# Optimization experiments

Hardware: AMD Instinct MI355X
Metric: run time of the kernel (lower is better)

Reference implementation:

```python
import jax, jax.numpy as jnp
import numpy as np

N, F, E = 1024, 32, 20


def setup_inputs() -> dict:
    key = jax.random.key(0)
    ks = jax.random.split(key, 18)
    f32 = jnp.float32
    nrm = lambda k, shape, s=1.0: (jax.random.normal(k, shape, f32) * s)
    scalar = nrm(ks[0], (N, 1, F))
    vector = nrm(ks[1], (N, 3, F))
    expansion = nrm(ks[2], (N, N, E))
    d = nrm(ks[3], (N, N, 3))
    direction = d / (jnp.linalg.norm(d, axis=-1, keepdims=True) + 1e-6)
    mask = (jax.random.uniform(ks[4], (N, N, 1)) < 0.9).astype(f32)
    w = 0.1  # weight scale
    return {
        "scalar": scalar, "vector": vector, "expansion": expansion,
        "direction": direction, "mask": mask,
        # message.msg_left: Linear(F,F) -> SiLU -> Linear(F,3F)
        "mL_w1": nrm(ks[5], (F, F), w), "mL_b1": jnp.zeros((F,), f32),
        "mL_w2": nrm(ks[6], (F, 3 * F), w), "mL_b2": jnp.zeros((3 * F,), f32),
        # message.msg_right: Linear(E, 3F)
        "mR_w": nrm(ks[7], (E, 3 * F), w), "mR_b": jnp.zeros((3 * F,), f32),
        # update.upd_right: Linear(2F,F) -> SiLU -> Linear(F,3F)
        "uR_w1": nrm(ks[8], (2 * F, F), w), "uR_b1": jnp.zeros((F,), f32),
        "uR_w2": nrm(ks[9], (F, 3 * F), w), "uR_b2": jnp.zeros((3 * F,), f32),
        # update.U / update.V: Linear(F,F,bias=False)
        "U_w": nrm(ks[10], (F, F), w),
        "V_w": nrm(ks[11], (F, F), w),
    }


def _message(s, v, expansion, direction, mask,
             mL_w1, mL_b1, mL_w2, mL_b2, mR_w, mR_b):
    # msg_left(s): [N,1,F] -> [N,1,3F]
    left = jax.nn.silu(s @ mL_w1 + mL_b1) @ mL_w2 + mL_b2
    # msg_right(expansion): [N,N,E] -> [N,N,3F] -> [N,N,1,3F]
    right = (expansion @ mR_w + mR_b)[..., None, :]
    prod = left * right                      # [N,N,1,3F]
    a, b, c = jnp.split(prod, 3, axis=-1)    # each [N,N,1,F]
    mask_ = mask[..., None]                  # [N,N,1,1]
    delta_s = jnp.sum(mask_ * b, axis=-3)    # [N,1,F]
    dv = v * a + direction[..., None] * c    # [N,N,3,F]
    delta_v = jnp.sum(mask_ * dv, axis=-3)   # [N,3,F]
    return delta_s, delta_v


def _update(scalar, vector, uR_w1, uR_b1, uR_w2, uR_b2, U_w, V_w):
    left = vector @ U_w                      # [N,3,F]
    right = vector @ V_w                     # [N,3,F]
    right_norm = jnp.linalg.norm(right, axis=-2, keepdims=True)   # [N,1,F]
    feats = jnp.concatenate((scalar, right_norm), axis=-1)        # [N,1,2F]
    feats = jax.nn.silu(feats @ uR_w1 + uR_b1) @ uR_w2 + uR_b2    # [N,1,3F]
    a, b, c = jnp.split(feats, 3, axis=-1)
    delta_v = a * left                                            # [N,3,F]
    inner = jnp.sum(left * right, axis=-2, keepdims=True)         # [N,1,F]
    delta_s = inner * b + c
    return delta_s, delta_v


def reference(scalar, vector, expansion, direction, mask,
              mL_w1, mL_b1, mL_w2, mL_b2, mR_w, mR_b,
              uR_w1, uR_b1, uR_w2, uR_b2, U_w, V_w):
    ds, dv = _message(scalar, vector, expansion, direction, mask,
                      mL_w1, mL_b1, mL_w2, mL_b2, mR_w, mR_b)
    scalar = scalar + ds
    vector = vector + dv
    ds, dv = _update(scalar, vector, uR_w1, uR_b1, uR_w2, uR_b2, U_w, V_w)
    return scalar + ds, vector + dv
```

## Files before the change

kernel.cpp:

```cpp
#include <hip/hip_runtime.h>
#include <hip/hip_bf16.h>
#include <math.h>

#define NN 1024
#define JS 64
#define NSL 16
#define PB 72
#define LP 40
#define WBUF 5376

typedef __attribute__((ext_vector_type(8))) short v8s;
typedef __attribute__((ext_vector_type(4))) float v4f;

#define MFMA(a, b, c) __builtin_amdgcn_mfma_f32_16x16x32_bf16((a), (b), (c), 0, 0, 0)

static __device__ __forceinline__ float silu_f(float x) {
    return x / (1.0f + __expf(-x));
}
static __device__ __forceinline__ unsigned short f2bf(float x) {
    __hip_bfloat16 h = __float2bfloat16(x);
    unsigned short u; __builtin_memcpy(&u, &h, 2); return u;
}
static __device__ __forceinline__ unsigned pack2bf(float lo, float hi) {
    __hip_bfloat162 h = __float22bfloat162_rn(make_float2(lo, hi));
    unsigned u; __builtin_memcpy(&u, &h, 4); return u;
}

extern "C" __global__ __launch_bounds__(128)
void node_kernel(const float* __restrict__ scalar,
                 const float* __restrict__ vector,
                 const float* __restrict__ mL_w1, const float* __restrict__ mL_b1,
                 const float* __restrict__ mL_w2, const float* __restrict__ mL_b2,
                 unsigned short* __restrict__ RT)
{
    const int j = blockIdx.x;
    const int t = threadIdx.x;
    __shared__ float ss[32], sh[32], sleft[96];

    if (t < 32) ss[t] = scalar[j * 32 + t];
    __syncthreads();
    if (t < 32) {
        float a = mL_b1[t];
        #pragma unroll
        for (int k = 0; k < 32; k++) a = fmaf(ss[k], mL_w1[k * 32 + t], a);
        sh[t] = silu_f(a);
    }
    __syncthreads();
    if (t < 96) {
        float a = mL_b2[t];
        #pragma unroll
        for (int k = 0; k < 32; k++) a = fmaf(sh[k], mL_w2[k * 96 + t], a);
        sleft[t] = a;
    }
    __syncthreads();
    for (int n = t; n < 160; n += 128) {
        float val;
        if (n < 32)        val = sleft[32 + n];
        else if (n < 128)  val = vector[j * 96 + (n - 32)] * sleft[(n - 32) & 31];
        else               val = sleft[64 + (n - 128)];
        RT[(size_t)n * NN + j] = f2bf(val);
    }
}

extern "C" __global__ __launch_bounds__(256, 3)
void edge_mfma_kernel(const float* __restrict__ expansion,
                      const float* __restrict__ direction,
                      const float* __restrict__ mask,
                      const float* __restrict__ mR_w, const float* __restrict__ mR_b,
                      const unsigned short* __restrict__ RT,
                      float* __restrict__ part)
{
    const int t = threadIdx.x;
    const int wave = t >> 6;
    const int lane = t & 63;
    const int lrow = lane & 15;
    const int quad = lane >> 4;
    const int jp = lane >> 2;
    const int g  = lane & 3;
    const int jl = jp * 2;

    const int bx = blockIdx.x;
    const int slice = bx & 15;
    const int i0 = (bx >> 4) * 4;
    const int j0s = slice * JS;

    __shared__ __align__(16) unsigned short BSm[160 * PB];
    __shared__ __align__(16) char Wm[4 * WBUF];

    for (int u = t; u < 160 * 8; u += 256) {
        const int row = u >> 3, seg = u & 7;
        *(uint4*)(BSm + row * PB + seg * 8) =
            *(const uint4*)(RT + (size_t)row * NN + j0s + seg * 8);
    }
    __syncthreads();

    char* wbase = Wm + wave * WBUF;
    const int ibase = i0 + (wave >> 1) * 2;

    if ((wave & 1) == 0) {
        unsigned short* L1 = (unsigned short*)wbase;
        float* S = (float*)wbase;

        v4f acc[16];
        #pragma unroll
        for (int q = 0; q < 16; ++q) acc[q] = (v4f){0.f, 0.f, 0.f, 0.f};

        float4 fa, fb, ca, cb; float m0, m1;
        {
            const size_t jg = (size_t)ibase * NN + j0s + jl;
            fa = *(const float4*)(expansion + jg * 20 + 4 * g);
            fb = *(const float4*)(expansion + (jg + 1) * 20 + 4 * g);
            ca = *(const float4*)(expansion + jg * 20 + 16);
            cb = *(const float4*)(expansion + (jg + 1) * 20 + 16);
            m0 = mask[jg]; m1 = mask[jg + 1];
        }

        for (int it = 0; it < 2; ++it) {
            const int i = ibase + it;
            for (int ch = 0; ch < 2; ++ch) {
                {
                    const float ea[4] = {fa.x, fa.y, fa.z, fa.w};
                    const float eb[4] = {fb.x, fb.y, fb.z, fb.w};
                    #pragma unroll
                    for (int k = 0; k < 4; ++k)
                        *(unsigned*)(L1 + (4 * g + k) * LP + jl) =
                            pack2bf(m0 * ea[k], m1 * eb[k]);
                    if (g == 3) {
                        const float caa[4] = {ca.x, ca.y, ca.z, ca.w};
                        const float cbb[4] = {cb.x, cb.y, cb.z, cb.w};
                        #pragma unroll
                        for (int k = 0; k < 4; ++k)
                            *(unsigned*)(L1 + (16 + k) * LP + jl) =
                                pack2bf(m0 * caa[k], m1 * cbb[k]);
                    }
                    if (g == 0) *(unsigned*)(L1 + 20 * LP + jl) = pack2bf(m0, m1);
                }
                {
                    const int u = it * 2 + ch;
                    const int un = (u < 3) ? u + 1 : 3;
                    const size_t jg =
                        (size_t)(ibase + (un >> 1)) * NN + j0s + (un & 1) * 32 + jl;
                    fa = *(const float4*)(expansion + jg * 20 + 4 * g);
                    fb = *(const float4*)(expansion + (jg + 1) * 20 + 4 * g);
                    ca = *(const float4*)(expansion + jg * 20 + 16);
                    cb = *(const float4*)(expansion + (jg + 1) * 20 + 16);
                    m0 = mask[jg]; m1 = mask[jg + 1];
                }
                {
                    const int ko = quad * 8;
                    const int kl = ch * 32 + ko;
                    const v8s a0 = *(const v8s*)(L1 + lrow * LP + ko);
                    const v8s a1 = *(const v8s*)(L1 + (16 + lrow) * LP + ko);
                    #pragma unroll
                    for (int nt = 0; nt < 8; ++nt) {
                        const v8s b = *(const v8s*)(BSm + (nt * 16 + lrow) * PB + kl);
                        acc[nt]     = MFMA(a0, b, acc[nt]);
                        acc[8 + nt] = MFMA(a1, b, acc[8 + nt]);
                    }
                }
            }
            float* pdst = part + ((size_t)i * NSL + slice) * 224;
            #pragma unroll
            for (int h = 0; h < 2; ++h) {
                #pragma unroll
                for (int mt = 0; mt < 2; ++mt)
                #pragma unroll
                for (int q = 0; q < 4; ++q)
                #pragma unroll
                for (int r = 0; r < 4; ++r) {
                    const int row = mt * 16 + quad * 4 + r;
                    if (row <= 20) S[row * 64 + q * 16 + lrow] = acc[mt * 8 + h * 4 + q][r];
                }
                const int col = h * 64 + lane;
                const int fw = (col < 32) ? (32 + col) : ((col - 32) & 31);
                float v = mR_b[fw] * S[20 * 64 + lane];
                #pragma unroll
                for (int e = 0; e < 20; ++e)
                    v = fmaf(mR_w[e * 96 + fw], S[e * 64 + lane], v);
                pdst[col] = v;
            }
            #pragma unroll
            for (int q = 0; q < 16; ++q) acc[q] = (v4f){0.f, 0.f, 0.f, 0.f};
        }
    } else {
        unsigned short* L2 = (unsigned short*)wbase;
        float* S = (float*)wbase;

        v4f acc[8];
        #pragma unroll
        for (int q = 0; q < 8; ++q) acc[q] = (v4f){0.f, 0.f, 0.f, 0.f};

        float4 fa, fb, ca, cb;
        float m0, m1, da0, da1, da2, db0, db1, db2;
        {
            const size_t jg = (size_t)ibase * NN + j0s + jl;
            fa = *(const float4*)(expansion + jg * 20 + 4 * g);
            fb = *(const float4*)(expansion + (jg + 1) * 20 + 4 * g);
            ca = *(const float4*)(expansion + jg * 20 + 16);
            cb = *(const float4*)(expansion + (jg + 1) * 20 + 16);
            m0 = mask[jg]; m1 = mask[jg + 1];
            da0 = direction[jg * 3 + 0]; da1 = direction[jg * 3 + 1]; da2 = direction[jg * 3 + 2];
            db0 = direction[(jg + 1) * 3 + 0]; db1 = direction[(jg + 1) * 3 + 1]; db2 = direction[(jg + 1) * 3 + 2];
        }

        for (int it = 0; it < 2; ++it) {
            const int i = ibase + it;
            for (int ch = 0; ch < 2; ++ch) {
                {
                    const float pa[3] = {m0 * da0, m0 * da1, m0 * da2};
                    const float pb[3] = {m1 * db0, m1 * db1, m1 * db2};
                    const float ea[4] = {fa.x, fa.y, fa.z, fa.w};
                    const float eb[4] = {fb.x, fb.y, fb.z, fb.w};
                    #pragma unroll
                    for (int d = 0; d < 3; ++d)
                        #pragma unroll
                        for (int k = 0; k < 4; ++k)
                            *(unsigned*)(L2 + (d * 20 + 4 * g + k) * LP + jl) =
                                pack2bf(pa[d] * ea[k], pb[d] * eb[k]);
                    if (g < 3) {
                        const float sa = (g == 0) ? pa[0] : ((g == 1) ? pa[1] : pa[2]);
                        const float sb = (g == 0) ? pb[0] : ((g == 1) ? pb[1] : pb[2]);
                        const float caa[4] = {ca.x, ca.y, ca.z, ca.w};
                        const float cbb[4] = {cb.x, cb.y, cb.z, cb.w};
                        #pragma unroll
                        for (int k = 0; k < 4; ++k)
                            *(unsigned*)(L2 + (g * 20 + 16 + k) * LP + jl) =
                                pack2bf(sa * caa[k], sb * cbb[k]);
                    } else {
                        *(unsigned*)(L2 + (60 + 0) * LP + jl) = pack2bf(pa[0], pb[0]);
                        *(unsigned*)(L2 + (60 + 1) * LP + jl) = pack2bf(pa[1], pb[1]);
                        *(unsigned*)(L2 + (60 + 2) * LP + jl) = pack2bf(pa[2], pb[2]);
                    }
                }
                {
                    const int u = it * 2 + ch;
                    const int un = (u < 3) ? u + 1 : 3;
                    const size_t jg =
                        (size_t)(ibase + (un >> 1)) * NN + j0s + (un & 1) * 32 + jl;
                    fa = *(const float4*)(expansion + jg * 20 + 4 * g);
                    fb = *(const float4*)(expansion + (jg + 1) * 20 + 4 * g);
                    ca = *(const float4*)(expansion + jg * 20 + 16);
                    cb = *(const float4*)(expansion + (jg + 1) * 20 + 16);
                    m0 = mask[jg]; m1 = mask[jg + 1];
                    da0 = direction[jg * 3 + 0]; da1 = direction[jg * 3 + 1]; da2 = direction[jg * 3 + 2];
                    db0 = direction[(jg + 1) * 3 + 0]; db1 = direction[(jg + 1) * 3 + 1]; db2 = direction[(jg + 1) * 3 + 2];
                }
                {
                    const int ko = quad * 8;
                    const int kl = ch * 32 + ko;
                    const v8s c0 = *(const v8s*)(L2 + (lrow) * LP + ko);
                    const v8s c1 = *(const v8s*)(L2 + (16 + lrow) * LP + ko);
                    const v8s c2 = *(const v8s*)(L2 + (32 + lrow) * LP + ko);
                    const v8s c3 = *(const v8s*)(L2 + (48 + lrow) * LP + ko);
                    const v8s b0 = *(const v8s*)(BSm + (128 + lrow) * PB + kl);
                    const v8s b1 = *(const v8s*)(BSm + (144 + lrow) * PB + kl);
                    acc[0] = MFMA(c0, b0, acc[0]); acc[1] = MFMA(c0, b1, acc[1]);
                    acc[2] = MFMA(c1, b0, acc[2]); acc[3] = MFMA(c1, b1, acc[3]);
                    acc[4] = MFMA(c2, b0, acc[4]); acc[5] = MFMA(c2, b1, acc[5]);
                    acc[6] = MFMA(c3, b0, acc[6]); acc[7] = MFMA(c3, b1, acc[7]);
                }
            }
            float* pdst = part + ((size_t)i * NSL + slice) * 224;
            #pragma unroll
            for (int h2 = 0; h2 < 2; ++h2) {
                #pragma unroll
                for (int mt = 0; mt < 4; ++mt)
                #pragma unroll
                for (int r = 0; r < 4; ++r) {
                    const int row = mt * 16 + quad * 4 + r;
                    if (row <= 62) S[row * 16 + lrow] = acc[mt * 2 + h2][r];
                }
                if (lane < 48) {
                    const int dd = lane >> 4, f16 = lane & 15;
                    const int f = h2 * 16 + f16;
                    float v = mR_b[64 + f] * S[(60 + dd) * 16 + f16];
                    #pragma unroll
                    for (int e = 0; e < 20; ++e)
                        v = fmaf(mR_w[e * 96 + 64 + f], S[(dd * 20 + e) * 16 + f16], v);
                    pdst[128 + dd * 32 + f] = v;
                }
            }
            #pragma unroll
            for (int q = 0; q < 8; ++q) acc[q] = (v4f){0.f, 0.f, 0.f, 0.f};
        }
    }
}

extern "C" __global__ __launch_bounds__(256)
void combine_kernel(const float* __restrict__ scalar,
                    const float* __restrict__ vector,
                    const float* __restrict__ uR_w1, const float* __restrict__ uR_b1,
                    const float* __restrict__ uR_w2, const float* __restrict__ uR_b2,
                    const float* __restrict__ U_w,  const float* __restrict__ V_w,
                    const float* __restrict__ part,
                    float* __restrict__ out)
{
    const int i = blockIdx.x;
    const int t = threadIdx.x;
    __shared__ float pcomb[224];
    __shared__ float snew[32], vnew[96];
    __shared__ float lU[96], rV[96], rnorm[32], h2[32], f2[96];

    if (t < 224) {
        const float* p = part + (size_t)i * NSL * 224 + t;
        float a = 0.f;
        #pragma unroll
        for (int s = 0; s < NSL; ++s) a += p[s * 224];
        pcomb[t] = a;
    }
    __syncthreads();

    if (t < 128) {
        const int d = t >> 5, ff = t & 31;
        if (d == 0) snew[ff] = scalar[i * 32 + ff] + pcomb[ff];
        else {
            const int q = t - 32;
            vnew[q] = vector[i * 96 + q] + pcomb[32 + q] + pcomb[128 + q];
        }
    }
    __syncthreads();

    if (t < 96) {
        const int d = t >> 5, ff = t & 31;
        float a = 0.0f;
        #pragma unroll
        for (int k = 0; k < 32; k++) a = fmaf(vnew[d * 32 + k], U_w[k * 32 + ff], a);
        lU[t] = a;
    } else if (t >= 128 && t < 224) {
        const int dt = t - 128, d = dt >> 5, ff = dt & 31;
        float a = 0.0f;
        #pragma unroll
        for (int k = 0; k < 32; k++) a = fmaf(vnew[d * 32 + k], V_w[k * 32 + ff], a);
        rV[dt] = a;
    }
    __syncthreads();
    if (t < 32) {
        const float a = rV[t] * rV[t] + rV[32 + t] * rV[32 + t] + rV[64 + t] * rV[64 + t];
        rnorm[t] = sqrtf(a);
    }
    __syncthreads();
    if (t < 32) {
        float a = uR_b1[t];
        #pragma unroll
        for (int k = 0; k < 32; k++) a = fmaf(snew[k],  uR_w1[k * 32 + t], a);
        #pragma unroll
        for (int k = 0; k < 32; k++) a = fmaf(rnorm[k], uR_w1[(32 + k) * 32 + t], a);
        h2[t] = silu_f(a);
    }
    __syncthreads();
    if (t < 96) {
        float a = uR_b2[t];
        #pragma unroll
        for (int k = 0; k < 32; k++) a = fmaf(h2[k], uR_w2[k * 96 + t], a);
        f2[t] = a;
    }
    __syncthreads();
    if (t < 32) {
        const float inner = lU[t] * rV[t] + lU[32 + t] * rV[32 + t] + lU[64 + t] * rV[64 + t];
        out[i * 32 + t] = snew[t] + inner * f2[32 + t] + f2[64 + t];
    } else if (t >= 64 && t < 160) {
        const int dt = t - 64, ff = dt & 31;
        out[32768 + i * 96 + dt] = vnew[dt] + f2[ff] * lU[dt];
    }
}

extern "C" void kernel_launch(void* const* d_in, const int* in_sizes, int n_in,
                              void* d_out, int out_size, void* d_ws, size_t ws_size,
                              hipStream_t stream) {
    const float* scalar    = (const float*)d_in[0];
    const float* vector    = (const float*)d_in[1];
    const float* expansion = (const float*)d_in[2];
    const float* direction = (const float*)d_in[3];
    const float* mask      = (const float*)d_in[4];
    const float* mL_w1     = (const float*)d_in[5];
    const float* mL_b1     = (const float*)d_in[6];
    const float* mL_w2     = (const float*)d_in[7];
    const float* mL_b2     = (const float*)d_in[8];
    const float* mR_w      = (const float*)d_in[9];
    const float* mR_b      = (const float*)d_in[10];
    const float* uR_w1     = (const float*)d_in[11];
    const float* uR_b1     = (const float*)d_in[12];
    const float* uR_w2     = (const float*)d_in[13];
    const float* uR_b2     = (const float*)d_in[14];
    const float* U_w       = (const float*)d_in[15];
    const float* V_w       = (const float*)d_in[16];
    float* out = (float*)d_out;

    unsigned short* RT = (unsigned short*)d_ws;
    float* part = (float*)((char*)d_ws + 160 * NN * 2);

    hipLaunchKernelGGL(node_kernel, dim3(NN), dim3(128), 0, stream,
                       scalar, vector, mL_w1, mL_b1, mL_w2, mL_b2, RT);
    hipLaunchKernelGGL(edge_mfma_kernel, dim3(4096), dim3(256), 0, stream,
                       expansion, direction, mask, mR_w, mR_b, RT, part);
    hipLaunchKernelGGL(combine_kernel, dim3(NN), dim3(256), 0, stream,
                       scalar, vector, uR_w1, uR_b1, uR_w2, uR_b2, U_w, V_w,
                       part, out);
}
```

Before: 211.0 us.

## Widen edge-kernel j-slice to 256 with one row per wave pair

Each block now covers 2 rows i (one per wave pair) across a 256-wide j slice instead of 4 rows across 64 columns. The RT tile is reloaded into shared memory four times per block, guarded by block-wide barriers. This cuts the number of partial slices from 16 to 4, which reduces partial-result writes and the epilogue projection work per edge, and halves the grid. The cost is extra barriers and serialized RT reloads inside the main loop, plus less total parallelism. The combine kernel must read NSL=4 partials through the shared macro.

```diff
diff --git a/kernel.cpp b/kernel.cpp
--- a/kernel.cpp
+++ b/kernel.cpp
@@ -3,8 +3,8 @@
 #include <math.h>
 
 #define NN 1024
-#define JS 64
-#define NSL 16
+#define JS 256
+#define NSL 4
 #define PB 72
 #define LP 40
 #define WBUF 5376
@@ -80,9 +80,9 @@
     const int jl = jp * 2;
 
     const int bx = blockIdx.x;
-    const int slice = bx & 15;
-    const int i0 = (bx >> 4) * 4;
-    const int j0s = slice * JS;
+    const int slice = bx & (NSL - 1);
+    const int j0 = slice * JS;
+    const int i = (bx >> 2) * 2 + (wave >> 1);
 
     __shared__ __align__(16) unsigned short BSm[160 * PB];
     __shared__ __align__(16) char Wm[4 * WBUF];
@@ -90,12 +90,11 @@
     for (int u = t; u < 160 * 8; u += 256) {
         const int row = u >> 3, seg = u & 7;
         *(uint4*)(BSm + row * PB + seg * 8) =
-            *(const uint4*)(RT + (size_t)row * NN + j0s + seg * 8);
+            *(const uint4*)(RT + (size_t)row * NN + j0 + seg * 8);
     }
     __syncthreads();
 
     char* wbase = Wm + wave * WBUF;
-    const int ibase = i0 + (wave >> 1) * 2;
 
     if ((wave & 1) == 0) {
         unsigned short* L1 = (unsigned short*)wbase;
@@ -107,7 +106,7 @@
 
         float4 fa, fb, ca, cb; float m0, m1;
         {
-            const size_t jg = (size_t)ibase * NN + j0s + jl;
+            const size_t jg = (size_t)i * NN + j0 + jl;
             fa = *(const float4*)(expansion + jg * 20 + 4 * g);
             fb = *(const float4*)(expansion + (jg + 1) * 20 + 4 * g);
             ca = *(const float4*)(expansion + jg * 20 + 16);
@@ -115,8 +114,8 @@
             m0 = mask[jg]; m1 = mask[jg + 1];
         }
 
-        for (int it = 0; it < 2; ++it) {
-            const int i = ibase + it;
+        for (int ss2 = 0; ss2 < 4; ++ss2) {
+            #pragma unroll
             for (int ch = 0; ch < 2; ++ch) {
                 {
                     const float ea[4] = {fa.x, fa.y, fa.z, fa.w};
@@ -136,10 +135,9 @@
                     if (g == 0) *(unsigned*)(L1 + 20 * LP + jl) = pack2bf(m0, m1);
                 }
                 {
-                    const int u = it * 2 + ch;
-                    const int un = (u < 3) ? u + 1 : 3;
-                    const size_t jg =
-                        (size_t)(ibase + (un >> 1)) * NN + j0s + (un & 1) * 32 + jl;
+                    const int u = ss2 * 2 + ch;
+                    const int un = (u < 7) ? u + 1 : 7;
+                    const size_t jg = (size_t)i * NN + j0 + un * 32 + jl;
                     fa = *(const float4*)(expansion + jg * 20 + 4 * g);
                     fb = *(const float4*)(expansion + (jg + 1) * 20 + 4 * g);
                     ca = *(const float4*)(expansion + jg * 20 + 16);
@@ -159,28 +157,36 @@
                     }
                 }
             }
-            float* pdst = part + ((size_t)i * NSL + slice) * 224;
-            #pragma unroll
-            for (int h = 0; h < 2; ++h) {
-                #pragma unroll
-                for (int mt = 0; mt < 2; ++mt)
-                #pragma unroll
-                for (int q = 0; q < 4; ++q)
-                #pragma unroll
-                for (int r = 0; r < 4; ++r) {
-                    const int row = mt * 16 + quad * 4 + r;
-                    if (row <= 20) S[row * 64 + q * 16 + lrow] = acc[mt * 8 + h * 4 + q][r];
-                }
-                const int col = h * 64 + lane;
-                const int fw = (col < 32) ? (32 + col) : ((col - 32) & 31);
-                float v = mR_b[fw] * S[20 * 64 + lane];
-                #pragma unroll
-                for (int e = 0; e < 20; ++e)
-                    v = fmaf(mR_w[e * 96 + fw], S[e * 64 + lane], v);
-                pdst[col] = v;
-            }
-            #pragma unroll
-            for (int q = 0; q < 16; ++q) acc[q] = (v4f){0.f, 0.f, 0.f, 0.f};
+            __syncthreads();
+            if (ss2 < 3) {
+                for (int u2 = t; u2 < 160 * 8; u2 += 256) {
+                    const int row = u2 >> 3, seg = u2 & 7;
+                    *(uint4*)(BSm + row * PB + seg * 8) =
+                        *(const uint4*)(RT + (size_t)row * NN + j0 + (ss2 + 1) * 64 + seg * 8);
+                }
+                __syncthreads();
+            }
+        }
+
+        float* pdst = part + ((size_t)i * NSL + slice) * 224;
+        #pragma unroll
+        for (int h = 0; h < 2; ++h) {
+            #pragma unroll
+            for (int mt = 0; mt < 2; ++mt)
+            #pragma unroll
+            for (int q = 0; q < 4; ++q)
+            #pragma unroll
+            for (int r = 0; r < 4; ++r) {
+                const int row = mt * 16 + quad * 4 + r;
+                if (row <= 20) S[row * 64 + q * 16 + lrow] = acc[mt * 8 + h * 4 + q][r];
+            }
+            const int col = h * 64 + lane;
+            const int fw = (col < 32) ? (32 + col) : ((col - 32) & 31);
+            float v = mR_b[fw] * S[20 * 64 + lane];
+            #pragma unroll
+            for (int e = 0; e < 20; ++e)
+                v = fmaf(mR_w[e * 96 + fw], S[e * 64 + lane], v);
+            pdst[col] = v;
         }
     } else {
         unsigned short* L2 = (unsigned short*)wbase;
@@ -193,7 +199,7 @@
         float4 fa, fb, ca, cb;
         float m0, m1, da0, da1, da2, db0, db1, db2;
         {
-            const size_t jg = (size_t)ibase * NN + j0s + jl;
+            const size_t jg = (size_t)i * NN + j0 + jl;
             fa = *(const float4*)(expansion + jg * 20 + 4 * g);
             fb = *(const float4*)(expansion + (jg + 1) * 20 + 4 * g);
             ca = *(const float4*)(expansion + jg * 20 + 16);
@@ -203,8 +209,8 @@
             db0 = direction[(jg + 1) * 3 + 0]; db1 = direction[(jg + 1) * 3 + 1]; db2 = direction[(jg + 1) * 3 + 2];
         }
 
-        for (int it = 0; it < 2; ++it) {
-            const int i = ibase + it;
+        for (int ss2 = 0; ss2 < 4; ++ss2) {
+            #pragma unroll
             for (int ch = 0; ch < 2; ++ch) {
                 {
                     const float pa[3] = {m0 * da0, m0 * da1, m0 * da2};
@@ -233,10 +239,9 @@
                     }
                 }
                 {
-                    const int u = it * 2 + ch;
-                    const int un = (u < 3) ? u + 1 : 3;
-                    const size_t jg =
-                        (size_t)(ibase + (un >> 1)) * NN + j0s + (un & 1) * 32 + jl;
+                    const int u = ss2 * 2 + ch;
+                    const int un = (u < 7) ? u + 1 : 7;
+                    const size_t jg = (size_t)i * NN + j0 + un * 32 + jl;
                     fa = *(const float4*)(expansion + jg * 20 + 4 * g);
                     fb = *(const float4*)(expansion + (jg + 1) * 20 + 4 * g);
                     ca = *(const float4*)(expansion + jg * 20 + 16);
@@ -260,28 +265,36 @@
                     acc[6] = MFMA(c3, b0, acc[6]); acc[7] = MFMA(c3, b1, acc[7]);
                 }
             }
-            float* pdst = part + ((size_t)i * NSL + slice) * 224;
-            #pragma unroll
-            for (int h2 = 0; h2 < 2; ++h2) {
+            __syncthreads();
+            if (ss2 < 3) {
+                for (int u2 = t; u2 < 160 * 8; u2 += 256) {
+                    const int row = u2 >> 3, seg = u2 & 7;
+                    *(uint4*)(BSm + row * PB + seg * 8) =
+                        *(const uint4*)(RT + (size_t)row * NN + j0 + (ss2 + 1) * 64 + seg * 8);
+                }
+                __syncthreads();
+            }
+        }
+
+        float* pdst = part + ((size_t)i * NSL + slice) * 224;
+        #pragma unroll
+        for (int h2 = 0; h2 < 2; ++h2) {
+            #pragma unroll
+            for (int mt = 0; mt < 4; ++mt)
+            #pragma unroll
+            for (int r = 0; r < 4; ++r) {
+                const int row = mt * 16 + quad * 4 + r;
+                if (row <= 62) S[row * 16 + lrow] = acc[mt * 2 + h2][r];
+            }
+            if (lane < 48) {
+                const int dd = lane >> 4, f16 = lane & 15;
+                const int f = h2 * 16 + f16;
+                float v = mR_b[64 + f] * S[(60 + dd) * 16 + f16];
                 #pragma unroll
-                for (int mt = 0; mt < 4; ++mt)
-                #pragma unroll
-                for (int r = 0; r < 4; ++r) {
-                    const int row = mt * 16 + quad * 4 + r;
-                    if (row <= 62) S[row * 16 + lrow] = acc[mt * 2 + h2][r];
-                }
-                if (lane < 48) {
-                    const int dd = lane >> 4, f16 = lane & 15;
-                    const int f = h2 * 16 + f16;
-                    float v = mR_b[64 + f] * S[(60 + dd) * 16 + f16];
-                    #pragma unroll
-                    for (int e = 0; e < 20; ++e)
-                        v = fmaf(mR_w[e * 96 + 64 + f], S[(dd * 20 + e) * 16 + f16], v);
-                    pdst[128 + dd * 32 + f] = v;
-                }
-            }
-            #pragma unroll
-            for (int q = 0; q < 8; ++q) acc[q] = (v4f){0.f, 0.f, 0.f, 0.f};
+                for (int e = 0; e < 20; ++e)
+                    v = fmaf(mR_w[e * 96 + 64 + f], S[(dd * 20 + e) * 16 + f16], v);
+                pdst[128 + dd * 32 + f] = v;
+            }
         }
     }
 }
@@ -391,7 +404,7 @@
 
     hipLaunchKernelGGL(node_kernel, dim3(NN), dim3(128), 0, stream,
                        scalar, vector, mL_w1, mL_b1, mL_w2, mL_b2, RT);
-    hipLaunchKernelGGL(edge_mfma_kernel, dim3(4096), dim3(256), 0, stream,
+    hipLaunchKernelGGL(edge_mfma_kernel, dim3(2048), dim3(256), 0, stream,
                        expansion, direction, mask, mR_w, mR_b, RT, part);
     hipLaunchKernelGGL(combine_kernel, dim3(NN), dim3(256), 0, stream,
                        scalar, vector, uR_w1, uR_b1, uR_w2, uR_b2, U_w, V_w,
```

Result: faster. 206.1 us (-2.3%).
